# Kernel tuning notes

Hardware: AMD Instinct MI355X
Metric: run time of the kernel (lower is better)

The kernel has to match this reference:

```python
import jax, jax.numpy as jnp
import numpy as np

N_NODES = 100000
NEG_SLOPE = 0.2  # PyG GATConv default negative_slope


def gat_layer(x, src, dst, W, a_src, a_dst, b):
    """PyG-style GATConv (eval mode: dropout = identity), concat=True.
    x: [N, F_in]; W: [F_in, H*C]; a_src/a_dst: [H, C]; b: [H*C].
    src/dst: [E] edge endpoints (messages flow src -> dst), self-loops included.
    """
    N = x.shape[0]
    H, C = a_src.shape
    h = (x @ W).reshape(N, H, C)                       # [N, H, C]
    al_s = jnp.sum(h * a_src, axis=-1)                 # [N, H]
    al_d = jnp.sum(h * a_dst, axis=-1)                 # [N, H]
    e = jax.nn.leaky_relu(al_s[src] + al_d[dst], NEG_SLOPE)  # [E, H]
    # softmax over incoming edges of each dst node (every node has a self-loop)
    m = jax.ops.segment_max(e, dst, num_segments=N)    # [N, H]
    ex = jnp.exp(e - m[dst])
    s = jax.ops.segment_sum(ex, dst, num_segments=N)   # [N, H]
    alpha = ex / s[dst]                                # [E, H]
    out = jax.ops.segment_sum(h[src] * alpha[:, :, None], dst, num_segments=N)
    return out.reshape(N, H * C) + b


def setup_inputs() -> dict:
    key = jax.random.key(0)
    ks = jax.random.split(key, 12)
    F_in, Hc, H, n_cls = 128, 32, 4, 3
    x = jax.random.normal(ks[0], (N_NODES, F_in), dtype=jnp.float32)
    edge_index = jax.random.randint(ks[1], (2, 1600000), 0, N_NODES, dtype=jnp.int64)
    sc1 = 1.0 / np.sqrt(F_in)
    sc2 = 1.0 / np.sqrt(Hc * H)
    return {
        "x": x,
        "edge_index": edge_index,
        "W1": jax.random.normal(ks[2], (F_in, H * Hc), dtype=jnp.float32) * sc1,
        "a1_src": jax.random.normal(ks[3], (H, Hc), dtype=jnp.float32) * sc1,
        "a1_dst": jax.random.normal(ks[4], (H, Hc), dtype=jnp.float32) * sc1,
        "b1": jnp.zeros((H * Hc,), dtype=jnp.float32),
        "W2": jax.random.normal(ks[5], (H * Hc, Hc), dtype=jnp.float32) * sc2,
        "a2_src": jax.random.normal(ks[6], (1, Hc), dtype=jnp.float32) * sc2,
        "a2_dst": jax.random.normal(ks[7], (1, Hc), dtype=jnp.float32) * sc2,
        "b2": jnp.zeros((Hc,), dtype=jnp.float32),
        "lin_W": jax.random.normal(ks[8], (Hc, n_cls), dtype=jnp.float32) * (1.0 / np.sqrt(Hc)),
        "lin_b": jnp.zeros((n_cls,), dtype=jnp.float32),
    }


def reference(x, edge_index, W1, a1_src, a1_dst, b1, W2, a2_src, a2_dst, b2, lin_W, lin_b):
    N = x.shape[0]
    loops = jnp.arange(N, dtype=edge_index.dtype)
    src = jnp.concatenate([edge_index[0], loops])
    dst = jnp.concatenate([edge_index[1], loops])
    h = jax.nn.elu(gat_layer(x, src, dst, W1, a1_src, a1_dst, b1))
    h = gat_layer(h, src, dst, W2, a2_src, a2_dst, b2)
    pooled = h.mean(axis=0, keepdims=True)             # batch=None path: [1, Hc]
    return jax.nn.softmax(pooled @ lin_W + lin_b, axis=1)
```

## Files before the change

### kernel.cpp

```cpp
#include <hip/hip_runtime.h>
#include <cstdint>
#include <cstddef>

static inline size_t align_up(size_t v, size_t a) { return (v + a - 1) & ~(a - 1); }

#define BCAP 3072

typedef __attribute__((ext_vector_type(8))) short short8;
typedef __attribute__((ext_vector_type(4))) float f32x4;
typedef __attribute__((ext_vector_type(2))) float f32x2;

__device__ inline unsigned short bf16_1(float x) {
  unsigned u = __float_as_uint(x);
  u += 0x7FFFu + ((u >> 16) & 1u);
  return (unsigned short)(u >> 16);
}
__device__ inline unsigned cvt_pk_bf16(float lo, float hi) {
  unsigned r;
  asm("v_cvt_pk_bf16_f32 %0, %1, %2" : "=v"(r) : "v"(lo), "v"(hi));
  return r;
}

__device__ inline unsigned char fp8_1(float x) {
  return (unsigned char)(__builtin_amdgcn_cvt_pk_fp8_f32(x, x, 0, false) & 0xFF);
}

__global__ void prep_kernel(const float* __restrict__ W1, const float* __restrict__ W2,
                            unsigned short* __restrict__ w1t, unsigned short* __restrict__ w2t,
                            int* __restrict__ fillB) {
  int t = blockIdx.x * 256 + threadIdx.x;
  if (t < 16384) {
    int c = t >> 7, k = t & 127;
    w1t[t] = bf16_1(W1[(size_t)k * 128 + c]);
  } else if (t < 20480) {
    int i = t - 16384;
    int c = i >> 7, k = i & 127;
    w2t[i] = bf16_1(W2[(size_t)k * 32 + c]);
  } else if (t < 21504) {
    fillB[t - 20480] = 0;
  }
}


__device__ inline int load_edge(const void* eidx, int is64, size_t idx) {
  if (is64) return (int)((const long long*)eidx)[idx];
  return ((const int*)eidx)[idx];
}

__global__ __launch_bounds__(256) void sortA_kernel(const void* eidx, int E,
                                                    int* __restrict__ fillB,
                                                    unsigned* __restrict__ packed, int NB) {
  __shared__ int hist[1024];
  __shared__ int loff[1024];
  __shared__ int lbase[1024];
  __shared__ int lcnt[1024];
  __shared__ unsigned sortedV[2048];
  __shared__ unsigned short sortedB[2048];
  __shared__ int s_is64;
  const int t = threadIdx.x;
  const int chunk0 = blockIdx.x * 2048;
  const int cntE = min(2048, E - chunk0);
  if (t == 0) s_is64 = 1;
  for (int i = t; i < 1024; i += 256) { hist[i] = 0; lcnt[i] = 0; }
  __syncthreads();
  {
    int nchk = min(cntE, 256);
    for (int i = t; i < nchk; i += 256)
      if (((const unsigned*)eidx)[2 * (size_t)(chunk0 + i) + 1] != 0u) s_is64 = 0;
  }
  __syncthreads();
  const int is64 = s_is64;
  int sv[8], dv[8];
#pragma unroll
  for (int it = 0; it < 8; ++it) {
    int li = it * 256 + t;
    if (li < cntE) {
      sv[it] = load_edge(eidx, is64, (size_t)chunk0 + li);
      dv[it] = load_edge(eidx, is64, (size_t)E + chunk0 + li);
      atomicAdd(&hist[dv[it] >> 7], 1);
    }
  }
  __syncthreads();
  for (int b = t; b < NB; b += 256) {
    int h = hist[b];
    if (h) lbase[b] = b * BCAP + atomicAdd(&fillB[b], h);
  }
  {
    int base = t * 4;
    int v[4]; int s = 0;
    __shared__ int sd[256];
#pragma unroll
    for (int j = 0; j < 4; ++j) { v[j] = hist[base + j]; s += v[j]; }
    sd[t] = s; __syncthreads();
    for (int off = 1; off < 256; off <<= 1) {
      int u = (t >= off) ? sd[t - off] : 0;
      __syncthreads();
      sd[t] += u;
      __syncthreads();
    }
    int run = sd[t] - s;
#pragma unroll
    for (int j = 0; j < 4; ++j) { loff[base + j] = run; run += v[j]; }
  }
  __syncthreads();
#pragma unroll
  for (int it = 0; it < 8; ++it) {
    int li = it * 256 + t;
    if (li < cntE) {
      int b = dv[it] >> 7;
      int r = atomicAdd(&lcnt[b], 1);
      int pos = loff[b] + r;
      sortedV[pos] = (unsigned)sv[it] | ((unsigned)(dv[it] & 127) << 20);
      sortedB[pos] = (unsigned short)b;
    }
  }
  __syncthreads();
  for (int li = t; li < cntE; li += 256) {
    int b = sortedB[li];
    packed[(size_t)lbase[b] + (li - loff[b])] = sortedV[li];
  }
}

__global__ __launch_bounds__(256) void buildCSR_kernel(const unsigned* __restrict__ packed,
                                                       const int* __restrict__ fillB,
                                                       int* __restrict__ rowbeg,
                                                       int* __restrict__ rowend,
                                                       int* __restrict__ csr, int N, int NB) {
  __shared__ int cnt[128], ex[128], fill[128];
  const int b = blockIdx.x;
  const int t = threadIdx.x;
  const int beg = b * BCAP;
  const int end = beg + fillB[b];
  const int node0 = b << 7;
  const int nn = min(128, N - node0);
  if (t < 128) { cnt[t] = 0; fill[t] = 0; }
  __syncthreads();
  for (int i = beg + t; i < end; i += 256) {
    int j = (packed[i] >> 20) & 127;
    atomicAdd(&cnt[j], 1);
  }
  __syncthreads();
  if (t < 128) ex[t] = cnt[t];
  __syncthreads();
  for (int off = 1; off < 128; off <<= 1) {
    int u = (t >= off && t < 128) ? ex[t - off] : 0;
    __syncthreads();
    if (t < 128) ex[t] += u;
    __syncthreads();
  }
  if (t < 128) ex[t] -= cnt[t];
  __syncthreads();
  if (t < nn) {
    rowbeg[node0 + t] = beg + ex[t];
    rowend[node0 + t] = beg + ex[t] + cnt[t];
  }
  for (int i = beg + t; i < end; i += 256) {
    unsigned v = packed[i];
    int j = (v >> 20) & 127;
    int r = atomicAdd(&fill[j], 1);
    csr[beg + ex[j] + r] = (int)(v & 0xFFFFFu);
  }
}

__global__ __launch_bounds__(256) void gemm1_mfma(
    const float* __restrict__ x, const unsigned short* __restrict__ w1t,
    const float* __restrict__ a1s, const float* __restrict__ a1d,
    unsigned char* __restrict__ h1f, float* __restrict__ al1s, float* __restrict__ al1d, int N) {
  __shared__ unsigned short sw[128 * 136];
  __shared__ unsigned short sx[64 * 136];
  unsigned char* ftile = (unsigned char*)sx;
  const int t = threadIdx.x;
  const int row0 = blockIdx.x * 64;
  for (int i = t; i < 4096; i += 256) {
    int c = i >> 5, k4 = (i & 31) * 4;
    *(ushort4*)&sw[c * 136 + k4] = *(const ushort4*)&w1t[c * 128 + k4];
  }
  for (int i = t; i < 2048; i += 256) {
    int r = i >> 5, c4 = (i & 31) * 4;
    float4 v = make_float4(0.f, 0.f, 0.f, 0.f);
    if (row0 + r < N) v = *(const float4*)(x + (size_t)(row0 + r) * 128 + c4);
    uint2 b;
    b.x = cvt_pk_bf16(v.x, v.y);
    b.y = cvt_pk_bf16(v.z, v.w);
    *(uint2*)&sx[r * 136 + c4] = b;
  }
  __syncthreads();
  const int lane = t & 63, wave = t >> 6;
  const int m = lane & 15, quad = lane >> 4;
  const unsigned short* arow = &sx[(wave * 16 + m) * 136];
  short8 A[4];
#pragma unroll
  for (int ks = 0; ks < 4; ++ks) A[ks] = *(const short8*)&arow[ks * 32 + quad * 8];
  __syncthreads();
  const int lrow = wave * 16 + quad * 4;
#pragma unroll
  for (int nt = 0; nt < 8; ++nt) {
    const unsigned short* brow = &sw[(nt * 16 + m) * 136];
    f32x4 acc = {0.f, 0.f, 0.f, 0.f};
#pragma unroll
    for (int ks = 0; ks < 4; ++ks) {
      short8 B = *(const short8*)&brow[ks * 32 + quad * 8];
      acc = __builtin_amdgcn_mfma_f32_16x16x32_bf16(A[ks], B, acc, 0, 0, 0);
    }
#pragma unroll
    for (int r = 0; r < 4; ++r)
      ftile[(lrow + r) * 128 + nt * 16 + m] = fp8_1(acc[r]);
  }
  __syncthreads();
#pragma unroll
  for (int it = 0; it < 2; ++it) {
    int row = it * 32 + (t >> 3);
    int chunk = t & 7;
    uint4 v = *(const uint4*)&ftile[row * 128 + chunk * 16];
    int grow = row0 + row;
    if (grow < N) *(uint4*)&h1f[(size_t)grow * 128 + chunk * 16] = v;
    unsigned w[4] = {v.x, v.y, v.z, v.w};
    float ps = 0.f, pd = 0.f;
    int cb = chunk * 16;
#pragma unroll
    for (int q = 0; q < 4; ++q) {
      f32x2 lo = __builtin_amdgcn_cvt_pk_f32_fp8((int)w[q], false);
      f32x2 hi = __builtin_amdgcn_cvt_pk_f32_fp8((int)w[q], true);
      int c = cb + q * 4;
      ps += lo[0] * a1s[c] + lo[1] * a1s[c + 1] + hi[0] * a1s[c + 2] + hi[1] * a1s[c + 3];
      pd += lo[0] * a1d[c] + lo[1] * a1d[c + 1] + hi[0] * a1d[c + 2] + hi[1] * a1d[c + 3];
    }
    ps += __shfl_xor(ps, 1); pd += __shfl_xor(pd, 1);
    if ((chunk & 1) == 0 && grow < N) {
      int head = chunk >> 1;
      al1s[(size_t)grow * 4 + head] = ps;
      al1d[(size_t)grow * 4 + head] = pd;
    }
  }
}

__global__ __launch_bounds__(256) void gemm2_mfma(
    const unsigned* __restrict__ houtb, const unsigned short* __restrict__ w2t,
    const float* __restrict__ a2s, const float* __restrict__ a2d,
    unsigned char* __restrict__ h2f, float* __restrict__ al2s, float* __restrict__ al2d, int N) {
  __shared__ unsigned short sw[32 * 136];
  __shared__ unsigned short sx[64 * 136];
  unsigned char* ftile = (unsigned char*)sx;
  const int t = threadIdx.x;
  const int row0 = blockIdx.x * 64;
  for (int i = t; i < 1024; i += 256) {
    int c = i >> 5, k4 = (i & 31) * 4;
    *(ushort4*)&sw[c * 136 + k4] = *(const ushort4*)&w2t[c * 128 + k4];
  }
  for (int i = t; i < 2048; i += 256) {
    int r = i >> 5, d2 = (i & 31) * 2;
    uint2 v = make_uint2(0u, 0u);
    if (row0 + r < N) v = *(const uint2*)(houtb + (size_t)(row0 + r) * 64 + d2);
    *(uint2*)&sx[r * 136 + d2 * 2] = v;
  }
  __syncthreads();
  const int lane = t & 63, wave = t >> 6;
  const int m = lane & 15, quad = lane >> 4;
  const unsigned short* arow = &sx[(wave * 16 + m) * 136];
  short8 A[4];
#pragma unroll
  for (int ks = 0; ks < 4; ++ks) A[ks] = *(const short8*)&arow[ks * 32 + quad * 8];
  __syncthreads();
  const int lrow = wave * 16 + quad * 4;
#pragma unroll
  for (int nt = 0; nt < 2; ++nt) {
    const unsigned short* brow = &sw[(nt * 16 + m) * 136];
    f32x4 acc = {0.f, 0.f, 0.f, 0.f};
#pragma unroll
    for (int ks = 0; ks < 4; ++ks) {
      short8 B = *(const short8*)&brow[ks * 32 + quad * 8];
      acc = __builtin_amdgcn_mfma_f32_16x16x32_bf16(A[ks], B, acc, 0, 0, 0);
    }
#pragma unroll
    for (int r = 0; r < 4; ++r)
      ftile[(lrow + r) * 32 + nt * 16 + m] = fp8_1(acc[r]);
  }
  __syncthreads();
  if (t < 128) {
    int row = t >> 1, chunk = t & 1;
    uint4 v = *(const uint4*)&ftile[row * 32 + chunk * 16];
    int grow = row0 + row;
    if (grow < N) *(uint4*)&h2f[(size_t)grow * 32 + chunk * 16] = v;
    unsigned w[4] = {v.x, v.y, v.z, v.w};
    float ps = 0.f, pd = 0.f;
    int cb = chunk * 16;
#pragma unroll
    for (int q = 0; q < 4; ++q) {
      f32x2 lo = __builtin_amdgcn_cvt_pk_f32_fp8((int)w[q], false);
      f32x2 hi = __builtin_amdgcn_cvt_pk_f32_fp8((int)w[q], true);
      int c = cb + q * 4;
      ps += lo[0] * a2s[c] + lo[1] * a2s[c + 1] + hi[0] * a2s[c + 2] + hi[1] * a2s[c + 3];
      pd += lo[0] * a2d[c] + lo[1] * a2d[c + 1] + hi[0] * a2d[c + 2] + hi[1] * a2d[c + 3];
    }
    ps += __shfl_xor(ps, 1); pd += __shfl_xor(pd, 1);
    if (chunk == 0 && grow < N) { al2s[grow] = ps; al2d[grow] = pd; }
  }
}

#define DEC8P(HV, EX)                                                       \
  {                                                                         \
    f32x2 _e2; _e2[0] = (EX); _e2[1] = (EX);                                \
    acc01 += __builtin_amdgcn_cvt_pk_f32_fp8((int)(HV).x, false) * _e2;     \
    acc23 += __builtin_amdgcn_cvt_pk_f32_fp8((int)(HV).x, true) * _e2;      \
    acc45 += __builtin_amdgcn_cvt_pk_f32_fp8((int)(HV).y, false) * _e2;     \
    acc67 += __builtin_amdgcn_cvt_pk_f32_fp8((int)(HV).y, true) * _e2;      \
    den += (EX);                                                            \
  }

__global__ __launch_bounds__(256) void agg1_kernel(
    const int* __restrict__ rowbeg, const int* __restrict__ rowend, const int* __restrict__ csr_src,
    const unsigned char* __restrict__ h1f,
    const float* __restrict__ al_s, const float* __restrict__ al_d,
    const float* __restrict__ b1, unsigned* __restrict__ houtb, int N) {
  int t = threadIdx.x;
  int d = (blockIdx.x * 256 + t) >> 6;
  if (d >= N) return;
  int lane = t & 63;
  int e_id = lane >> 4;
  unsigned c8 = (unsigned)(lane & 15);
  unsigned head = c8 >> 2;
  const unsigned boff = c8 * 8u;
  const float ald = al_d[(unsigned)d * 4u + head];
  const int beg = __builtin_amdgcn_readfirstlane(rowbeg[d]);
  const int end = __builtin_amdgcn_readfirstlane(rowend[d]);
  int idx0 = beg + e_id;
  int idx1 = idx0 + 4;
  int sj0 = (idx0 < end) ? csr_src[(unsigned)idx0] : d;
  int sj1 = (idx1 < end) ? csr_src[(unsigned)idx1] : d;
  f32x2 acc01 = {0.f, 0.f}, acc23 = {0.f, 0.f}, acc45 = {0.f, 0.f}, acc67 = {0.f, 0.f};
  float den = 0.f;
  {
    float e = al_s[(unsigned)d * 4u + head] + ald;
    e = fmaxf(e, 0.2f * e);
    float ex = (e_id == 0) ? __expf(e) : 0.f;
    uint2 hv = *(const uint2*)(h1f + (((unsigned)d << 7) | boff));
    DEC8P(hv, ex);
  }
  for (int i = beg; i < end; i += 8) {
    const int cidx0 = idx0, cidx1 = idx1;
    const int csj0 = sj0, csj1 = sj1;
    float as0 = al_s[(unsigned)csj0 * 4u + head];
    float as1 = al_s[(unsigned)csj1 * 4u + head];
    uint2 hv0 = *(const uint2*)(h1f + (((unsigned)csj0 << 7) | boff));
    uint2 hv1 = *(const uint2*)(h1f + (((unsigned)csj1 << 7) | boff));
    idx0 += 8; idx1 += 8;
    sj0 = (idx0 < end) ? csr_src[(unsigned)idx0] : d;
    sj1 = (idx1 < end) ? csr_src[(unsigned)idx1] : d;
    float e0 = as0 + ald;
    e0 = fmaxf(e0, 0.2f * e0);
    float ex0 = __expf(e0);
    if (cidx0 >= end) ex0 = 0.f;
    float e1 = as1 + ald;
    e1 = fmaxf(e1, 0.2f * e1);
    float ex1 = __expf(e1);
    if (cidx1 >= end) ex1 = 0.f;
    DEC8P(hv0, ex0);
    DEC8P(hv1, ex1);
  }
  float a0 = acc01[0], a1 = acc01[1], a2 = acc23[0], a3 = acc23[1];
  float a4 = acc45[0], a5 = acc45[1], a6 = acc67[0], a7 = acc67[1];
  a0 += __shfl_xor(a0, 16); a1 += __shfl_xor(a1, 16);
  a2 += __shfl_xor(a2, 16); a3 += __shfl_xor(a3, 16);
  a4 += __shfl_xor(a4, 16); a5 += __shfl_xor(a5, 16);
  a6 += __shfl_xor(a6, 16); a7 += __shfl_xor(a7, 16);
  den += __shfl_xor(den, 16);
  a0 += __shfl_xor(a0, 32); a1 += __shfl_xor(a1, 32);
  a2 += __shfl_xor(a2, 32); a3 += __shfl_xor(a3, 32);
  a4 += __shfl_xor(a4, 32); a5 += __shfl_xor(a5, 32);
  a6 += __shfl_xor(a6, 32); a7 += __shfl_xor(a7, 32);
  den += __shfl_xor(den, 32);
  float inv = __builtin_amdgcn_rcpf(den);
  float p0 = e_id == 0 ? a0 : e_id == 1 ? a2 : e_id == 2 ? a4 : a6;
  float p1 = e_id == 0 ? a1 : e_id == 1 ? a3 : e_id == 2 ? a5 : a7;
  float2 bv = *(const float2*)(b1 + 8 * c8 + 2 * e_id);
  float o0 = p0 * inv + bv.x;
  float o1 = p1 * inv + bv.y;
  o0 = o0 > 0.f ? o0 : __expf(o0) - 1.f;
  o1 = o1 > 0.f ? o1 : __expf(o1) - 1.f;
  houtb[(unsigned)d * 64u + 4u * c8 + (unsigned)e_id] = cvt_pk_bf16(o0, o1);
}

__global__ __launch_bounds__(256) void agg2_kernel(
    const int* __restrict__ rowbeg, const int* __restrict__ rowend, const int* __restrict__ csr_src,
    const unsigned char* __restrict__ h2f,
    const float* __restrict__ al_s, const float* __restrict__ al_d,
    float* __restrict__ partial, int N) {
  __shared__ float sp[16 * 32];
  int t = threadIdx.x;
  int l16 = t & 15;
  int slot = t >> 4;
  int node = (blockIdx.x * 256 + t) >> 4;
  int e_id = l16 >> 2;
  unsigned c8 = (unsigned)(l16 & 3);
  const unsigned boff = c8 * 8u;
  float po0 = 0.f, po1 = 0.f;
  if (node < N) {
    const float ald = al_d[node];
    const int beg = rowbeg[node], end = rowend[node];
    int idx0 = beg + e_id;
    int idx1 = idx0 + 4;
    int sj0 = (idx0 < end) ? csr_src[(unsigned)idx0] : node;
    int sj1 = (idx1 < end) ? csr_src[(unsigned)idx1] : node;
    float self_as = al_s[node];
    uint2 self_hv = *(const uint2*)(h2f + (((unsigned)node << 5) | boff));
    idx0 += 8; idx1 += 8;
    int nsj0 = (idx0 < end) ? csr_src[(unsigned)idx0] : node;
    int nsj1 = (idx1 < end) ? csr_src[(unsigned)idx1] : node;
    float as0 = al_s[(unsigned)sj0];
    float as1 = al_s[(unsigned)sj1];
    uint2 hv0 = *(const uint2*)(h2f + (((unsigned)sj0 << 5) | boff));
    uint2 hv1 = *(const uint2*)(h2f + (((unsigned)sj1 << 5) | boff));
    f32x2 acc01 = {0.f, 0.f}, acc23 = {0.f, 0.f}, acc45 = {0.f, 0.f}, acc67 = {0.f, 0.f};
    float den = 0.f;
    {
      float e = self_as + ald;
      e = fmaxf(e, 0.2f * e);
      float ex = (e_id == 0) ? __expf(e) : 0.f;
      DEC8P(self_hv, ex);
    }
    for (int i = beg; i < end; i += 8) {
      idx0 += 8; idx1 += 8;
      int nnsj0 = (idx0 < end) ? csr_src[(unsigned)idx0] : node;
      int nnsj1 = (idx1 < end) ? csr_src[(unsigned)idx1] : node;
      float nas0 = al_s[(unsigned)nsj0];
      float nas1 = al_s[(unsigned)nsj1];
      uint2 nhv0 = *(const uint2*)(h2f + (((unsigned)nsj0 << 5) | boff));
      uint2 nhv1 = *(const uint2*)(h2f + (((unsigned)nsj1 << 5) | boff));
      int cix0 = i + e_id;
      int cix1 = cix0 + 4;
      float e0 = as0 + ald;
      e0 = fmaxf(e0, 0.2f * e0);
      float ex0 = __expf(e0);
      if (cix0 >= end) ex0 = 0.f;
      float e1 = as1 + ald;
      e1 = fmaxf(e1, 0.2f * e1);
      float ex1 = __expf(e1);
      if (cix1 >= end) ex1 = 0.f;
      DEC8P(hv0, ex0);
      DEC8P(hv1, ex1);
      as0 = nas0; as1 = nas1; hv0 = nhv0; hv1 = nhv1;
      nsj0 = nnsj0; nsj1 = nnsj1;
    }
    float a0 = acc01[0], a1 = acc01[1], a2 = acc23[0], a3 = acc23[1];
    float a4 = acc45[0], a5 = acc45[1], a6 = acc67[0], a7 = acc67[1];
    a0 += __shfl_xor(a0, 4); a1 += __shfl_xor(a1, 4);
    a2 += __shfl_xor(a2, 4); a3 += __shfl_xor(a3, 4);
    a4 += __shfl_xor(a4, 4); a5 += __shfl_xor(a5, 4);
    a6 += __shfl_xor(a6, 4); a7 += __shfl_xor(a7, 4);
    den += __shfl_xor(den, 4);
    a0 += __shfl_xor(a0, 8); a1 += __shfl_xor(a1, 8);
    a2 += __shfl_xor(a2, 8); a3 += __shfl_xor(a3, 8);
    a4 += __shfl_xor(a4, 8); a5 += __shfl_xor(a5, 8);
    a6 += __shfl_xor(a6, 8); a7 += __shfl_xor(a7, 8);
    den += __shfl_xor(den, 8);
    float inv = __builtin_amdgcn_rcpf(den);
    float p0 = e_id == 0 ? a0 : e_id == 1 ? a2 : e_id == 2 ? a4 : a6;
    float p1 = e_id == 0 ? a1 : e_id == 1 ? a3 : e_id == 2 ? a5 : a7;
    po0 = p0 * inv; po1 = p1 * inv;
  }
  *(float2*)&sp[slot * 32 + 8 * c8 + 2 * e_id] = make_float2(po0, po1);
  __syncthreads();
  if (t < 32) {
    float s = 0.f;
#pragma unroll
    for (int j = 0; j < 16; ++j) s += sp[j * 32 + t];
    partial[(size_t)blockIdx.x * 32 + t] = s;
  }
}

__global__ __launch_bounds__(256) void reduce_kernel(
    const float* __restrict__ partial, int nb, float* __restrict__ partial2) {
  __shared__ float sp[8 * 32];
  int t = threadIdx.x;
  int slot = t >> 5, c = t & 31;
  int row0 = blockIdx.x * 8 + slot;
  float s = 0.f;
  for (int i = row0; i < nb; i += 1024) s += partial[(size_t)i * 32 + c];
  sp[slot * 32 + c] = s;
  __syncthreads();
  if (t < 32) {
    float tot = 0.f;
#pragma unroll
    for (int j = 0; j < 8; ++j) tot += sp[j * 32 + t];
    partial2[(size_t)blockIdx.x * 32 + t] = tot;
  }
}

__global__ void final_kernel(const float* __restrict__ partial2, int nb,
                             const float* __restrict__ b2, const float* __restrict__ linW,
                             const float* __restrict__ linb, float* __restrict__ out, int N) {
  __shared__ float sd[256];
  __shared__ float pooled[32];
  int t = threadIdx.x;
  int c = t & 31, g = t >> 5;
  float s = 0.f;
  for (int i = g; i < nb; i += 8) s += partial2[(size_t)i * 32 + c];
  sd[t] = s; __syncthreads();
  if (t < 32) {
    float tot = 0.f;
#pragma unroll
    for (int j = 0; j < 8; ++j) tot += sd[j * 32 + t];
    pooled[t] = tot / (float)N + b2[t];
  }
  __syncthreads();
  if (t == 0) {
    float lg[3];
    for (int j = 0; j < 3; ++j) lg[j] = linb[j];
    for (int cc = 0; cc < 32; ++cc)
      for (int j = 0; j < 3; ++j) lg[j] += pooled[cc] * linW[cc * 3 + j];
    float m = fmaxf(lg[0], fmaxf(lg[1], lg[2]));
    float e0 = __expf(lg[0] - m), e1 = __expf(lg[1] - m), e2 = __expf(lg[2] - m);
    float inv = 1.f / (e0 + e1 + e2);
    out[0] = e0 * inv; out[1] = e1 * inv; out[2] = e2 * inv;
  }
}

extern "C" void kernel_launch(void* const* d_in, const int* in_sizes, int n_in,
                              void* d_out, int out_size, void* d_ws, size_t ws_size,
                              hipStream_t stream) {
  const float* x    = (const float*)d_in[0];
  const void*  eidx = d_in[1];
  const float* W1   = (const float*)d_in[2];
  const float* a1s  = (const float*)d_in[3];
  const float* a1d  = (const float*)d_in[4];
  const float* b1   = (const float*)d_in[5];
  const float* W2   = (const float*)d_in[6];
  const float* a2s  = (const float*)d_in[7];
  const float* a2d  = (const float*)d_in[8];
  const float* b2   = (const float*)d_in[9];
  const float* linW = (const float*)d_in[10];
  const float* linb = (const float*)d_in[11];
  float* out = (float*)d_out;

  const int N = in_sizes[0] / 128;
  const int E = in_sizes[1] / 2;
  const int NB = (N + 127) >> 7;

  char* ws = (char*)d_ws;
  size_t off = 0;
  auto alloc = [&](size_t bytes) -> void* {
    size_t o = off;
    off = align_up(off + bytes, 256);
    return (void*)(ws + o);
  };
  int* fillB  = (int*)alloc((size_t)1024 * sizeof(int));
  int* rowbeg = (int*)alloc((size_t)N * sizeof(int));
  int* rowend = (int*)alloc((size_t)N * sizeof(int));
  unsigned* packed = (unsigned*)alloc((size_t)NB * BCAP * sizeof(unsigned));
  int* csr    = (int*)alloc((size_t)NB * BCAP * sizeof(int));
  float* al1s = (float*)alloc((size_t)N * 4 * sizeof(float));
  float* al1d = (float*)alloc((size_t)N * 4 * sizeof(float));
  float* al2s = (float*)alloc((size_t)N * sizeof(float));
  float* al2d = (float*)alloc((size_t)N * sizeof(float));
  unsigned short* w1t = (unsigned short*)alloc(16384 * sizeof(unsigned short));
  unsigned short* w2t = (unsigned short*)alloc(4096 * sizeof(unsigned short));
  unsigned char* h1f  = (unsigned char*)alloc((size_t)N * 128);
  unsigned* houtb = (unsigned*)alloc((size_t)N * 64 * sizeof(unsigned));
  unsigned char* h2f  = (unsigned char*)alloc((size_t)N * 32);
  const int nAggBlocks = (N + 15) / 16;
  float* partial  = (float*)alloc((size_t)nAggBlocks * 32 * sizeof(float));
  float* partial2 = (float*)alloc((size_t)128 * 32 * sizeof(float));

  prep_kernel<<<84, 256, 0, stream>>>(W1, W2, w1t, w2t, fillB);

  sortA_kernel<<<(E + 2047) / 2048, 256, 0, stream>>>(eidx, E, fillB, packed, NB);
  buildCSR_kernel<<<NB, 256, 0, stream>>>(packed, fillB, rowbeg, rowend, csr, N, NB);

  const int gemmBlocks = (N + 63) / 64;
  gemm1_mfma<<<gemmBlocks, 256, 0, stream>>>(x, w1t, a1s, a1d, h1f, al1s, al1d, N);
  agg1_kernel<<<(N * 64 + 255) / 256, 256, 0, stream>>>(
      rowbeg, rowend, csr, h1f, al1s, al1d, b1, houtb, N);
  gemm2_mfma<<<gemmBlocks, 256, 0, stream>>>(houtb, w2t, a2s, a2d, h2f, al2s, al2d, N);
  agg2_kernel<<<(N * 16 + 255) / 256, 256, 0, stream>>>(
      rowbeg, rowend, csr, h2f, al2s, al2d, partial, N);
  reduce_kernel<<<128, 256, 0, stream>>>(partial, nAggBlocks, partial2);
  final_kernel<<<1, 256, 0, stream>>>(partial2, 128, b2, linW, linb, out, N);
}
```

Baseline: 264.7 us.

## Pad CSR rows to multiples of 8 with sentinel node, use exp2 with prescaled logits

Result: slower. 275.6 us (+4.1%).

```diff
diff --git a/kernel.cpp b/kernel.cpp
--- a/kernel.cpp
+++ b/kernel.cpp
@@ -4,7 +4,8 @@
 
 static inline size_t align_up(size_t v, size_t a) { return (v + a - 1) & ~(a - 1); }
 
-#define BCAP 3072
+#define BCAP 3456
+#define LOG2E 1.4426950408889634f
 
 typedef __attribute__((ext_vector_type(8))) short short8;
 typedef __attribute__((ext_vector_type(4))) float f32x4;
@@ -27,7 +28,9 @@
 
 __global__ void prep_kernel(const float* __restrict__ W1, const float* __restrict__ W2,
                             unsigned short* __restrict__ w1t, unsigned short* __restrict__ w2t,
-                            int* __restrict__ fillB) {
+                            int* __restrict__ fillB,
+                            unsigned* __restrict__ h1f_row_n, unsigned* __restrict__ h2f_row_n,
+                            float* __restrict__ al1s_row_n, float* __restrict__ al2s_n) {
   int t = blockIdx.x * 256 + threadIdx.x;
   if (t < 16384) {
     int c = t >> 7, k = t & 127;
@@ -38,6 +41,14 @@
     w2t[i] = bf16_1(W2[(size_t)k * 32 + c]);
   } else if (t < 21504) {
     fillB[t - 20480] = 0;
+  } else if (t < 21536) {
+    h1f_row_n[t - 21504] = 0u;
+  } else if (t < 21544) {
+    h2f_row_n[t - 21536] = 0u;
+  } else if (t < 21548) {
+    al1s_row_n[t - 21544] = -INFINITY;
+  } else if (t < 21549) {
+    al2s_n[0] = -INFINITY;
   }
 }
 
@@ -126,7 +137,7 @@
                                                        int* __restrict__ rowbeg,
                                                        int* __restrict__ rowend,
                                                        int* __restrict__ csr, int N, int NB) {
-  __shared__ int cnt[128], ex[128], fill[128];
+  __shared__ int cnt[128], pc[128], ex[128], fill[128];
   const int b = blockIdx.x;
   const int t = threadIdx.x;
   const int beg = b * BCAP;
@@ -140,7 +151,7 @@
     atomicAdd(&cnt[j], 1);
   }
   __syncthreads();
-  if (t < 128) ex[t] = cnt[t];
+  if (t < 128) { pc[t] = (cnt[t] + 7) & ~7; ex[t] = pc[t]; }
   __syncthreads();
   for (int off = 1; off < 128; off <<= 1) {
     int u = (t >= off && t < 128) ? ex[t - off] : 0;
@@ -148,11 +159,13 @@
     if (t < 128) ex[t] += u;
     __syncthreads();
   }
-  if (t < 128) ex[t] -= cnt[t];
+  if (t < 128) ex[t] -= pc[t];
   __syncthreads();
   if (t < nn) {
-    rowbeg[node0 + t] = beg + ex[t];
-    rowend[node0 + t] = beg + ex[t] + cnt[t];
+    int rb = beg + ex[t];
+    rowbeg[node0 + t] = rb;
+    rowend[node0 + t] = rb + pc[t];
+    for (int s = rb + cnt[t]; s < rb + pc[t]; ++s) csr[s] = N;
   }
   for (int i = beg + t; i < end; i += 256) {
     unsigned v = packed[i];
@@ -228,8 +241,8 @@
     ps += __shfl_xor(ps, 1); pd += __shfl_xor(pd, 1);
     if ((chunk & 1) == 0 && grow < N) {
       int head = chunk >> 1;
-      al1s[(size_t)grow * 4 + head] = ps;
-      al1d[(size_t)grow * 4 + head] = pd;
+      al1s[(size_t)grow * 4 + head] = ps * LOG2E;
+      al1d[(size_t)grow * 4 + head] = pd * LOG2E;
     }
   }
 }
@@ -293,7 +306,10 @@
       pd += lo[0] * a2d[c] + lo[1] * a2d[c + 1] + hi[0] * a2d[c + 2] + hi[1] * a2d[c + 3];
     }
     ps += __shfl_xor(ps, 1); pd += __shfl_xor(pd, 1);
-    if (chunk == 0 && grow < N) { al2s[grow] = ps; al2d[grow] = pd; }
+    if (chunk == 0 && grow < N) {
+      al2s[grow] = ps * LOG2E;
+      al2d[grow] = pd * LOG2E;
+    }
   }
 }
 
@@ -325,35 +341,32 @@
   const int end = __builtin_amdgcn_readfirstlane(rowend[d]);
   int idx0 = beg + e_id;
   int idx1 = idx0 + 4;
-  int sj0 = (idx0 < end) ? csr_src[(unsigned)idx0] : d;
-  int sj1 = (idx1 < end) ? csr_src[(unsigned)idx1] : d;
+  int sj0 = csr_src[(unsigned)idx0];
+  int sj1 = csr_src[(unsigned)idx1];
   f32x2 acc01 = {0.f, 0.f}, acc23 = {0.f, 0.f}, acc45 = {0.f, 0.f}, acc67 = {0.f, 0.f};
   float den = 0.f;
   {
     float e = al_s[(unsigned)d * 4u + head] + ald;
     e = fmaxf(e, 0.2f * e);
-    float ex = (e_id == 0) ? __expf(e) : 0.f;
+    float ex = (e_id == 0) ? exp2f(e) : 0.f;
     uint2 hv = *(const uint2*)(h1f + (((unsigned)d << 7) | boff));
     DEC8P(hv, ex);
   }
   for (int i = beg; i < end; i += 8) {
-    const int cidx0 = idx0, cidx1 = idx1;
     const int csj0 = sj0, csj1 = sj1;
     float as0 = al_s[(unsigned)csj0 * 4u + head];
     float as1 = al_s[(unsigned)csj1 * 4u + head];
     uint2 hv0 = *(const uint2*)(h1f + (((unsigned)csj0 << 7) | boff));
     uint2 hv1 = *(const uint2*)(h1f + (((unsigned)csj1 << 7) | boff));
     idx0 += 8; idx1 += 8;
-    sj0 = (idx0 < end) ? csr_src[(unsigned)idx0] : d;
-    sj1 = (idx1 < end) ? csr_src[(unsigned)idx1] : d;
+    sj0 = csr_src[(unsigned)idx0];
+    sj1 = csr_src[(unsigned)idx1];
     float e0 = as0 + ald;
     e0 = fmaxf(e0, 0.2f * e0);
-    float ex0 = __expf(e0);
-    if (cidx0 >= end) ex0 = 0.f;
+    float ex0 = exp2f(e0);
     float e1 = as1 + ald;
     e1 = fmaxf(e1, 0.2f * e1);
-    float ex1 = __expf(e1);
-    if (cidx1 >= end) ex1 = 0.f;
+    float ex1 = exp2f(e1);
     DEC8P(hv0, ex0);
     DEC8P(hv1, ex1);
   }
@@ -399,13 +412,13 @@
     const int beg = rowbeg[node], end = rowend[node];
     int idx0 = beg + e_id;
     int idx1 = idx0 + 4;
-    int sj0 = (idx0 < end) ? csr_src[(unsigned)idx0] : node;
-    int sj1 = (idx1 < end) ? csr_src[(unsigned)idx1] : node;
+    int sj0 = csr_src[(unsigned)idx0];
+    int sj1 = csr_src[(unsigned)idx1];
     float self_as = al_s[node];
     uint2 self_hv = *(const uint2*)(h2f + (((unsigned)node << 5) | boff));
     idx0 += 8; idx1 += 8;
-    int nsj0 = (idx0 < end) ? csr_src[(unsigned)idx0] : node;
-    int nsj1 = (idx1 < end) ? csr_src[(unsigned)idx1] : node;
+    int nsj0 = csr_src[(unsigned)idx0];
+    int nsj1 = csr_src[(unsigned)idx1];
     float as0 = al_s[(unsigned)sj0];
     float as1 = al_s[(unsigned)sj1];
     uint2 hv0 = *(const uint2*)(h2f + (((unsigned)sj0 << 5) | boff));
@@ -415,27 +428,23 @@
     {
       float e = self_as + ald;
       e = fmaxf(e, 0.2f * e);
-      float ex = (e_id == 0) ? __expf(e) : 0.f;
+      float ex = (e_id == 0) ? exp2f(e) : 0.f;
       DEC8P(self_hv, ex);
     }
     for (int i = beg; i < end; i += 8) {
       idx0 += 8; idx1 += 8;
-      int nnsj0 = (idx0 < end) ? csr_src[(unsigned)idx0] : node;
-      int nnsj1 = (idx1 < end) ? csr_src[(unsigned)idx1] : node;
+      int nnsj0 = csr_src[(unsigned)idx0];
+      int nnsj1 = csr_src[(unsigned)idx1];
       float nas0 = al_s[(unsigned)nsj0];
       float nas1 = al_s[(unsigned)nsj1];
       uint2 nhv0 = *(const uint2*)(h2f + (((unsigned)nsj0 << 5) | boff));
       uint2 nhv1 = *(const uint2*)(h2f + (((unsigned)nsj1 << 5) | boff));
-      int cix0 = i + e_id;
-      int cix1 = cix0 + 4;
       float e0 = as0 + ald;
       e0 = fmaxf(e0, 0.2f * e0);
-      float ex0 = __expf(e0);
-      if (cix0 >= end) ex0 = 0.f;
+      float ex0 = exp2f(e0);
       float e1 = as1 + ald;
       e1 = fmaxf(e1, 0.2f * e1);
-      float ex1 = __expf(e1);
-      if (cix1 >= end) ex1 = 0.f;
+      float ex1 = exp2f(e1);
       DEC8P(hv0, ex0);
       DEC8P(hv1, ex1);
       as0 = nas0; as1 = nas1; hv0 = nhv0; hv1 = nhv1;
@@ -548,20 +557,23 @@
   int* rowend = (int*)alloc((size_t)N * sizeof(int));
   unsigned* packed = (unsigned*)alloc((size_t)NB * BCAP * sizeof(unsigned));
   int* csr    = (int*)alloc((size_t)NB * BCAP * sizeof(int));
-  float* al1s = (float*)alloc((size_t)N * 4 * sizeof(float));
+  float* al1s = (float*)alloc((size_t)(N + 1) * 4 * sizeof(float));
   float* al1d = (float*)alloc((size_t)N * 4 * sizeof(float));
-  float* al2s = (float*)alloc((size_t)N * sizeof(float));
+  float* al2s = (float*)alloc((size_t)(N + 1) * sizeof(float));
   float* al2d = (float*)alloc((size_t)N * sizeof(float));
   unsigned short* w1t = (unsigned short*)alloc(16384 * sizeof(unsigned short));
   unsigned short* w2t = (unsigned short*)alloc(4096 * sizeof(unsigned short));
-  unsigned char* h1f  = (unsigned char*)alloc((size_t)N * 128);
+  unsigned char* h1f  = (unsigned char*)alloc((size_t)(N + 1) * 128);
   unsigned* houtb = (unsigned*)alloc((size_t)N * 64 * sizeof(unsigned));
-  unsigned char* h2f  = (unsigned char*)alloc((size_t)N * 32);
+  unsigned char* h2f  = (unsigned char*)alloc((size_t)(N + 1) * 32);
   const int nAggBlocks = (N + 15) / 16;
   float* partial  = (float*)alloc((size_t)nAggBlocks * 32 * sizeof(float));
   float* partial2 = (float*)alloc((size_t)128 * 32 * sizeof(float));
 
-  prep_kernel<<<84, 256, 0, stream>>>(W1, W2, w1t, w2t, fillB);
+  prep_kernel<<<85, 256, 0, stream>>>(W1, W2, w1t, w2t, fillB,
+                                      (unsigned*)(h1f + (size_t)N * 128),
+                                      (unsigned*)(h2f + (size_t)N * 32),
+                                      al1s + (size_t)N * 4, al2s + N);
 
   sortA_kernel<<<(E + 2047) / 2048, 256, 0, stream>>>(eidx, E, fillB, packed, NB);
   buildCSR_kernel<<<NB, 256, 0, stream>>>(packed, fillB, rowbeg, rowend, csr, N, NB);
```

## Merge edge bucket sort and first GEMM into one heterogeneous launch

Applied to the files above, without the earlier changes.

After: 261.2 us. No clear change (-1.3%).

```diff
diff --git a/kernel.cpp b/kernel.cpp
--- a/kernel.cpp
+++ b/kernel.cpp
@@ -41,35 +41,36 @@
   }
 }
 
-
 __device__ inline int load_edge(const void* eidx, int is64, size_t idx) {
   if (is64) return (int)((const long long*)eidx)[idx];
   return ((const int*)eidx)[idx];
 }
 
-__global__ __launch_bounds__(256) void sortA_kernel(const void* eidx, int E,
-                                                    int* __restrict__ fillB,
-                                                    unsigned* __restrict__ packed, int NB) {
-  __shared__ int hist[1024];
-  __shared__ int loff[1024];
-  __shared__ int lbase[1024];
-  __shared__ int lcnt[1024];
-  __shared__ unsigned sortedV[2048];
-  __shared__ unsigned short sortedB[2048];
-  __shared__ int s_is64;
+
+__device__ void sortA_body(char* smem, const void* eidx, int E,
+                           int* __restrict__ fillB, unsigned* __restrict__ packed,
+                           int NB, int bid) {
+  int* hist = (int*)smem;
+  int* loff = hist + 1024;
+  int* lbase = loff + 1024;
+  int* lcnt = lbase + 1024;
+  unsigned* sortedV = (unsigned*)(lcnt + 1024);
+  unsigned short* sortedB = (unsigned short*)(sortedV + 2048);
+  int* sd = (int*)(sortedB + 2048);
+  int* s_is64 = sd + 256;
   const int t = threadIdx.x;
-  const int chunk0 = blockIdx.x * 2048;
+  const int chunk0 = bid * 2048;
   const int cntE = min(2048, E - chunk0);
-  if (t == 0) s_is64 = 1;
+  if (t == 0) *s_is64 = 1;
   for (int i = t; i < 1024; i += 256) { hist[i] = 0; lcnt[i] = 0; }
   __syncthreads();
   {
     int nchk = min(cntE, 256);
     for (int i = t; i < nchk; i += 256)
-      if (((const unsigned*)eidx)[2 * (size_t)(chunk0 + i) + 1] != 0u) s_is64 = 0;
-  }
-  __syncthreads();
-  const int is64 = s_is64;
+      if (((const unsigned*)eidx)[2 * (size_t)(chunk0 + i) + 1] != 0u) *s_is64 = 0;
+  }
+  __syncthreads();
+  const int is64 = *s_is64;
   int sv[8], dv[8];
 #pragma unroll
   for (int it = 0; it < 8; ++it) {
@@ -88,7 +89,6 @@
   {
     int base = t * 4;
     int v[4]; int s = 0;
-    __shared__ int sd[256];
 #pragma unroll
     for (int j = 0; j < 4; ++j) { v[j] = hist[base + j]; s += v[j]; }
     sd[t] = s; __syncthreads();
@@ -118,6 +118,95 @@
   for (int li = t; li < cntE; li += 256) {
     int b = sortedB[li];
     packed[(size_t)lbase[b] + (li - loff[b])] = sortedV[li];
+  }
+}
+
+__device__ void gemm1_body(char* smem,
+    const float* __restrict__ x, const unsigned short* __restrict__ w1t,
+    const float* __restrict__ a1s, const float* __restrict__ a1d,
+    unsigned char* __restrict__ h1f, float* __restrict__ al1s, float* __restrict__ al1d,
+    int N, int bid) {
+  unsigned short* sw = (unsigned short*)smem;
+  unsigned short* sx = sw + 128 * 136;
+  unsigned char* ftile = (unsigned char*)sx;
+  const int t = threadIdx.x;
+  const int row0 = bid * 64;
+  for (int i = t; i < 4096; i += 256) {
+    int c = i >> 5, k4 = (i & 31) * 4;
+    *(ushort4*)&sw[c * 136 + k4] = *(const ushort4*)&w1t[c * 128 + k4];
+  }
+  for (int i = t; i < 2048; i += 256) {
+    int r = i >> 5, c4 = (i & 31) * 4;
+    float4 v = make_float4(0.f, 0.f, 0.f, 0.f);
+    if (row0 + r < N) v = *(const float4*)(x + (size_t)(row0 + r) * 128 + c4);
+    uint2 b;
+    b.x = cvt_pk_bf16(v.x, v.y);
+    b.y = cvt_pk_bf16(v.z, v.w);
+    *(uint2*)&sx[r * 136 + c4] = b;
+  }
+  __syncthreads();
+  const int lane = t & 63, wave = t >> 6;
+  const int m = lane & 15, quad = lane >> 4;
+  const unsigned short* arow = &sx[(wave * 16 + m) * 136];
+  short8 A[4];
+#pragma unroll
+  for (int ks = 0; ks < 4; ++ks) A[ks] = *(const short8*)&arow[ks * 32 + quad * 8];
+  __syncthreads();
+  const int lrow = wave * 16 + quad * 4;
+#pragma unroll
+  for (int nt = 0; nt < 8; ++nt) {
+    const unsigned short* brow = &sw[(nt * 16 + m) * 136];
+    f32x4 acc = {0.f, 0.f, 0.f, 0.f};
+#pragma unroll
+    for (int ks = 0; ks < 4; ++ks) {
+      short8 B = *(const short8*)&brow[ks * 32 + quad * 8];
+      acc = __builtin_amdgcn_mfma_f32_16x16x32_bf16(A[ks], B, acc, 0, 0, 0);
+    }
+#pragma unroll
+    for (int r = 0; r < 4; ++r)
+      ftile[(lrow + r) * 128 + nt * 16 + m] = fp8_1(acc[r]);
+  }
+  __syncthreads();
+#pragma unroll
+  for (int it = 0; it < 2; ++it) {
+    int row = it * 32 + (t >> 3);
+    int chunk = t & 7;
+    uint4 v = *(const uint4*)&ftile[row * 128 + chunk * 16];
+    int grow = row0 + row;
+    if (grow < N) *(uint4*)&h1f[(size_t)grow * 128 + chunk * 16] = v;
+    unsigned w[4] = {v.x, v.y, v.z, v.w};
+    float ps = 0.f, pd = 0.f;
+    int cb = chunk * 16;
+#pragma unroll
+    for (int q = 0; q < 4; ++q) {
+      f32x2 lo = __builtin_amdgcn_cvt_pk_f32_fp8((int)w[q], false);
+      f32x2 hi = __builtin_amdgcn_cvt_pk_f32_fp8((int)w[q], true);
+      int c = cb + q * 4;
+      ps += lo[0] * a1s[c] + lo[1] * a1s[c + 1] + hi[0] * a1s[c + 2] + hi[1] * a1s[c + 3];
+      pd += lo[0] * a1d[c] + lo[1] * a1d[c + 1] + hi[0] * a1d[c + 2] + hi[1] * a1d[c + 3];
+    }
+    ps += __shfl_xor(ps, 1); pd += __shfl_xor(pd, 1);
+    if ((chunk & 1) == 0 && grow < N) {
+      int head = chunk >> 1;
+      al1s[(size_t)grow * 4 + head] = ps;
+      al1d[(size_t)grow * 4 + head] = pd;
+    }
+  }
+}
+
+__global__ __launch_bounds__(256) void fused_sort_gemm1(
+    const void* eidx, int E, int* __restrict__ fillB, unsigned* __restrict__ packed,
+    int NB, int NBs,
+    const float* __restrict__ x, const unsigned short* __restrict__ w1t,
+    const float* __restrict__ a1s, const float* __restrict__ a1d,
+    unsigned char* __restrict__ h1f, float* __restrict__ al1s, float* __restrict__ al1d,
+    int N) {
+  __shared__ __align__(16) char smem[52224];
+  int bid = blockIdx.x;
+  if (bid < NBs) {
+    sortA_body(smem, eidx, E, fillB, packed, NB, bid);
+  } else {
+    gemm1_body(smem, x, w1t, a1s, a1d, h1f, al1s, al1d, N, bid - NBs);
   }
 }
 
@@ -159,78 +248,6 @@
     int j = (v >> 20) & 127;
     int r = atomicAdd(&fill[j], 1);
     csr[beg + ex[j] + r] = (int)(v & 0xFFFFFu);
-  }
-}
-
-__global__ __launch_bounds__(256) void gemm1_mfma(
-    const float* __restrict__ x, const unsigned short* __restrict__ w1t,
-    const float* __restrict__ a1s, const float* __restrict__ a1d,
-    unsigned char* __restrict__ h1f, float* __restrict__ al1s, float* __restrict__ al1d, int N) {
-  __shared__ unsigned short sw[128 * 136];
-  __shared__ unsigned short sx[64 * 136];
-  unsigned char* ftile = (unsigned char*)sx;
-  const int t = threadIdx.x;
-  const int row0 = blockIdx.x * 64;
-  for (int i = t; i < 4096; i += 256) {
-    int c = i >> 5, k4 = (i & 31) * 4;
-    *(ushort4*)&sw[c * 136 + k4] = *(const ushort4*)&w1t[c * 128 + k4];
-  }
-  for (int i = t; i < 2048; i += 256) {
-    int r = i >> 5, c4 = (i & 31) * 4;
-    float4 v = make_float4(0.f, 0.f, 0.f, 0.f);
-    if (row0 + r < N) v = *(const float4*)(x + (size_t)(row0 + r) * 128 + c4);
-    uint2 b;
-    b.x = cvt_pk_bf16(v.x, v.y);
-    b.y = cvt_pk_bf16(v.z, v.w);
-    *(uint2*)&sx[r * 136 + c4] = b;
-  }
-  __syncthreads();
-  const int lane = t & 63, wave = t >> 6;
-  const int m = lane & 15, quad = lane >> 4;
-  const unsigned short* arow = &sx[(wave * 16 + m) * 136];
-  short8 A[4];
-#pragma unroll
-  for (int ks = 0; ks < 4; ++ks) A[ks] = *(const short8*)&arow[ks * 32 + quad * 8];
-  __syncthreads();
-  const int lrow = wave * 16 + quad * 4;
-#pragma unroll
-  for (int nt = 0; nt < 8; ++nt) {
-    const unsigned short* brow = &sw[(nt * 16 + m) * 136];
-    f32x4 acc = {0.f, 0.f, 0.f, 0.f};
-#pragma unroll
-    for (int ks = 0; ks < 4; ++ks) {
-      short8 B = *(const short8*)&brow[ks * 32 + quad * 8];
-      acc = __builtin_amdgcn_mfma_f32_16x16x32_bf16(A[ks], B, acc, 0, 0, 0);
-    }
-#pragma unroll
-    for (int r = 0; r < 4; ++r)
-      ftile[(lrow + r) * 128 + nt * 16 + m] = fp8_1(acc[r]);
-  }
-  __syncthreads();
-#pragma unroll
-  for (int it = 0; it < 2; ++it) {
-    int row = it * 32 + (t >> 3);
-    int chunk = t & 7;
-    uint4 v = *(const uint4*)&ftile[row * 128 + chunk * 16];
-    int grow = row0 + row;
-    if (grow < N) *(uint4*)&h1f[(size_t)grow * 128 + chunk * 16] = v;
-    unsigned w[4] = {v.x, v.y, v.z, v.w};
-    float ps = 0.f, pd = 0.f;
-    int cb = chunk * 16;
-#pragma unroll
-    for (int q = 0; q < 4; ++q) {
-      f32x2 lo = __builtin_amdgcn_cvt_pk_f32_fp8((int)w[q], false);
-      f32x2 hi = __builtin_amdgcn_cvt_pk_f32_fp8((int)w[q], true);
-      int c = cb + q * 4;
-      ps += lo[0] * a1s[c] + lo[1] * a1s[c + 1] + hi[0] * a1s[c + 2] + hi[1] * a1s[c + 3];
-      pd += lo[0] * a1d[c] + lo[1] * a1d[c + 1] + hi[0] * a1d[c + 2] + hi[1] * a1d[c + 3];
-    }
-    ps += __shfl_xor(ps, 1); pd += __shfl_xor(pd, 1);
-    if ((chunk & 1) == 0 && grow < N) {
-      int head = chunk >> 1;
-      al1s[(size_t)grow * 4 + head] = ps;
-      al1d[(size_t)grow * 4 + head] = pd;
-    }
   }
 }
 
@@ -563,11 +580,12 @@
 
   prep_kernel<<<84, 256, 0, stream>>>(W1, W2, w1t, w2t, fillB);
 
-  sortA_kernel<<<(E + 2047) / 2048, 256, 0, stream>>>(eidx, E, fillB, packed, NB);
+  const int NBs = (E + 2047) / 2048;
+  const int gemmBlocks = (N + 63) / 64;
+  fused_sort_gemm1<<<NBs + gemmBlocks, 256, 0, stream>>>(
+      eidx, E, fillB, packed, NB, NBs, x, w1t, a1s, a1d, h1f, al1s, al1d, N);
+
   buildCSR_kernel<<<NB, 256, 0, stream>>>(packed, fillB, rowbeg, rowend, csr, N, NB);
-
-  const int gemmBlocks = (N + 63) / 64;
-  gemm1_mfma<<<gemmBlocks, 256, 0, stream>>>(x, w1t, a1s, a1d, h1f, al1s, al1d, N);
   agg1_kernel<<<(N * 64 + 255) / 256, 256, 0, stream>>>(
       rowbeg, rowend, csr, h1f, al1s, al1d, b1, houtb, N);
   gemm2_mfma<<<gemmBlocks, 256, 0, stream>>>(houtb, w2t, a2s, a2d, h2f, al2s, al2d, N);
```
